# Kernel tuning notes

Hardware: AMD Instinct MI355X
Metric: run time of the kernel (lower is better)

The kernel has to match this reference:

```python
import jax, jax.numpy as jnp
import numpy as np

DELTA = 0.1      # delta from __init__
LN_EPS = 1e-5    # torch LayerNorm default eps

B, IN, OUT, E = 256, 512, 512, 256


def setup_inputs() -> dict:
    key = jax.random.key(0)
    ks = jax.random.split(key, 6)
    return {
        "x": jax.random.normal(ks[0], (B, IN), dtype=jnp.float32),
        # nn.init.normal_(std=0.1), shape (out_features, in_features)
        "weights": 0.1 * jax.random.normal(ks[1], (OUT, IN), dtype=jnp.float32),
        # frozen predicate embeddings (in_features, embedding_dim)
        "pred_emb": jax.random.normal(ks[2], (IN, E), dtype=jnp.float32),
        # nn.Linear(E, OUT): weight (OUT, E), bias (OUT,)
        "attn_w": jax.random.uniform(ks[3], (OUT, E), dtype=jnp.float32,
                                      minval=-1.0, maxval=1.0) / np.sqrt(E),
        "attn_b": jax.random.uniform(ks[4], (OUT,), dtype=jnp.float32,
                                      minval=-1.0, maxval=1.0) / np.sqrt(E),
        # nn.LayerNorm(OUT)
        "ln_g": jnp.ones((OUT,), dtype=jnp.float32),
        "ln_b": jnp.zeros((OUT,), dtype=jnp.float32),
    }


def _layernorm(s, g, b):
    mu = s.mean(axis=-1, keepdims=True)
    var = ((s - mu) ** 2).mean(axis=-1, keepdims=True)
    return (s - mu) * jax.lax.rsqrt(var + LN_EPS) * g + b


def reference(x, weights, pred_emb, attn_w, attn_b, ln_g, ln_b):
    # semantic attention gate: batch-invariant, compute once -> (IN, OUT)
    scores = pred_emb @ attn_w.T + attn_b                    # (IN, OUT)
    sig = jax.nn.sigmoid(_layernorm(scores, ln_g, ln_b))     # (IN, OUT)

    xe = x[:, :, None]                                       # (B, IN, 1)
    wt = weights.T[None]                                     # (1, IN, OUT)
    # abs_weight * attn_adjusted, fused elementwise -> (B, IN, OUT)
    aw = jnp.abs(xe * wt) * (sig[None] * xe)

    bias = aw.max(axis=1) - aw.sum(axis=1)                   # CONJUNCTION: max - sum
    return x @ weights.T + DELTA * bias                      # (B, OUT)
```

## Files before the change

kernel.cpp:

```cpp
#include <hip/hip_runtime.h>
#include <hip/hip_bf16.h>
#include <math.h>

#define B_   256
#define IN_  512
#define OUT_ 512
#define E_   256
#define DELTA_ 0.1f
#define LN_EPS_ 1e-5f

#define K1_R 2

__global__ __launch_bounds__(256)
void k1_scores_ln_sig(const float* __restrict__ pred_emb,
                      const float* __restrict__ attn_w,
                      const float* __restrict__ attn_b,
                      const float* __restrict__ ln_g,
                      const float* __restrict__ ln_b,
                      const float* __restrict__ weights,
                      float2* __restrict__ wv) {
    __shared__ float pe[K1_R][E_];
    __shared__ float red[4][K1_R][2];
    __shared__ float smu[K1_R], srs[K1_R];

    const int t    = threadIdx.x;
    const int lane = t & 63;
    const int wid  = t >> 6;
    const int i0   = blockIdx.x * K1_R;

    #pragma unroll
    for (int r = 0; r < K1_R; ++r)
        pe[r][t] = pred_emb[(size_t)(i0 + r) * E_ + t];
    __syncthreads();

    const float4 (*pe4)[E_ / 4] = reinterpret_cast<const float4(*)[E_ / 4]>(pe);

    float acc[K1_R][2];
    #pragma unroll
    for (int oo = 0; oo < 2; ++oo) {
        const int o = t + oo * 256;
        const float4* wrow = reinterpret_cast<const float4*>(attn_w + (size_t)o * E_);
        float a0 = 0.f, a1 = 0.f;
        #pragma unroll 8
        for (int e4 = 0; e4 < E_ / 4; ++e4) {
            float4 w4 = wrow[e4];
            float4 p0 = pe4[0][e4];
            float4 p1 = pe4[1][e4];
            a0 += p0.x * w4.x + p0.y * w4.y + p0.z * w4.z + p0.w * w4.w;
            a1 += p1.x * w4.x + p1.y * w4.y + p1.z * w4.z + p1.w * w4.w;
        }
        const float bo = attn_b[o];
        acc[0][oo] = a0 + bo;
        acc[1][oo] = a1 + bo;
    }

    #pragma unroll
    for (int r = 0; r < K1_R; ++r) {
        float s1 = acc[r][0] + acc[r][1];
        float s2 = acc[r][0] * acc[r][0] + acc[r][1] * acc[r][1];
        #pragma unroll
        for (int off = 32; off > 0; off >>= 1) {
            s1 += __shfl_down(s1, off);
            s2 += __shfl_down(s2, off);
        }
        if (lane == 0) { red[wid][r][0] = s1; red[wid][r][1] = s2; }
    }
    __syncthreads();
    if (t < K1_R) {
        float s1 = red[0][t][0] + red[1][t][0] + red[2][t][0] + red[3][t][0];
        float s2 = red[0][t][1] + red[1][t][1] + red[2][t][1] + red[3][t][1];
        float mu  = s1 / (float)OUT_;
        float var = s2 / (float)OUT_ - mu * mu;
        smu[t] = mu;
        srs[t] = rsqrtf(var + LN_EPS_);
    }
    __syncthreads();

    #pragma unroll
    for (int oo = 0; oo < 2; ++oo) {
        const int o = t + oo * 256;
        const float g  = ln_g[o];
        const float bb = ln_b[o];
        #pragma unroll
        for (int r = 0; r < K1_R; ++r) {
            float z  = (acc[r][oo] - smu[r]) * srs[r] * g + bb;
            float sg = 1.f / (1.f + expf(-z));
            float w  = weights[(size_t)o * IN_ + (i0 + r)];
            wv[(size_t)(i0 + r) * OUT_ + o] = make_float2(w, fabsf(w) * sg);
        }
    }
}

#define K2_SK 4
#define K2_CH 128
#define K2_BO (B_ * OUT_)

__global__ __launch_bounds__(256)
void k2_partials(const float* __restrict__ x,
                 const float2* __restrict__ wv,
                 float* __restrict__ plin,
                 float* __restrict__ pmax) {
    __shared__ float4 xs4[32 * 33];
    __shared__ float2 ws2[K2_CH * 17];

    const int t  = threadIdx.x;
    const int ot = t & 15;
    const int bl = t >> 4;
    const int o0 = blockIdx.x * 16;
    const int b0 = blockIdx.y * 32;
    const int sk = blockIdx.z;
    const int i0 = sk * K2_CH;

    #pragma unroll
    for (int k = 0; k < 4; ++k) {
        int p    = t + k * 256;
        int row  = p >> 5;
        int col4 = p & 31;
        xs4[row * 33 + col4] = reinterpret_cast<const float4*>(
            x + (size_t)(b0 + row) * IN_ + i0)[col4];
    }
    #pragma unroll
    for (int k = 0; k < 8; ++k) {
        int r = (t >> 4) + 16 * k;
        int c = t & 15;
        ws2[r * 17 + c] = wv[(size_t)(i0 + r) * OUT_ + o0 + c];
    }
    __syncthreads();

    const int o = o0 + ot;
    float da = 0.f, sa = 0.f, ma = -INFINITY;
    float db = 0.f, sb = 0.f, mb = -INFINITY;

    #pragma unroll 4
    for (int i4 = 0; i4 < K2_CH / 4; ++i4) {
        float4 xa = xs4[bl * 33 + i4];
        float4 xb = xs4[(bl + 16) * 33 + i4];
        float4 ua = make_float4(xa.x * fabsf(xa.x), xa.y * fabsf(xa.y),
                                xa.z * fabsf(xa.z), xa.w * fabsf(xa.w));
        float4 ub = make_float4(xb.x * fabsf(xb.x), xb.y * fabsf(xb.y),
                                xb.z * fabsf(xb.z), xb.w * fabsf(xb.w));
        float2 w0 = ws2[(4 * i4 + 0) * 17 + ot];
        float2 w1 = ws2[(4 * i4 + 1) * 17 + ot];
        float2 w2 = ws2[(4 * i4 + 2) * 17 + ot];
        float2 w3 = ws2[(4 * i4 + 3) * 17 + ot];
        float p;
        da = fmaf(xa.x, w0.x, da); p = ua.x * w0.y; sa += p; ma = fmaxf(ma, p);
        db = fmaf(xb.x, w0.x, db); p = ub.x * w0.y; sb += p; mb = fmaxf(mb, p);
        da = fmaf(xa.y, w1.x, da); p = ua.y * w1.y; sa += p; ma = fmaxf(ma, p);
        db = fmaf(xb.y, w1.x, db); p = ub.y * w1.y; sb += p; mb = fmaxf(mb, p);
        da = fmaf(xa.z, w2.x, da); p = ua.z * w2.y; sa += p; ma = fmaxf(ma, p);
        db = fmaf(xb.z, w2.x, db); p = ub.z * w2.y; sb += p; mb = fmaxf(mb, p);
        da = fmaf(xa.w, w3.x, da); p = ua.w * w3.y; sa += p; ma = fmaxf(ma, p);
        db = fmaf(xb.w, w3.x, db); p = ub.w * w3.y; sb += p; mb = fmaxf(mb, p);
    }

    const size_t boa = (size_t)(b0 + bl) * OUT_ + o;
    const size_t bob = boa + (size_t)16 * OUT_;
    plin[(size_t)sk * K2_BO + boa] = da - DELTA_ * sa;
    pmax[(size_t)sk * K2_BO + boa] = ma;
    plin[(size_t)sk * K2_BO + bob] = db - DELTA_ * sb;
    pmax[(size_t)sk * K2_BO + bob] = mb;
}

__global__ __launch_bounds__(256)
void k3_combine(const float* __restrict__ plin,
                const float* __restrict__ pmax,
                float* __restrict__ out) {
    const int g = blockIdx.x * 256 + threadIdx.x;
    float l = plin[g] + plin[K2_BO + g] + plin[2 * K2_BO + g] + plin[3 * K2_BO + g];
    float m = fmaxf(fmaxf(pmax[g], pmax[K2_BO + g]),
                    fmaxf(pmax[2 * K2_BO + g], pmax[3 * K2_BO + g]));
    out[g] = l + DELTA_ * m;
}

extern "C" void kernel_launch(void* const* d_in, const int* in_sizes, int n_in,
                              void* d_out, int out_size, void* d_ws, size_t ws_size,
                              hipStream_t stream) {
    const float* x        = (const float*)d_in[0];
    const float* weights  = (const float*)d_in[1];
    const float* pred_emb = (const float*)d_in[2];
    const float* attn_w   = (const float*)d_in[3];
    const float* attn_b   = (const float*)d_in[4];
    const float* ln_g     = (const float*)d_in[5];
    const float* ln_b     = (const float*)d_in[6];
    float* out = (float*)d_out;

    float2* wv   = (float2*)d_ws;
    float*  plin = (float*)d_ws + 2 * (size_t)IN_ * OUT_;
    float*  pmax = plin + (size_t)K2_SK * K2_BO;

    k1_scores_ln_sig<<<IN_ / K1_R, 256, 0, stream>>>(
        pred_emb, attn_w, attn_b, ln_g, ln_b, weights, wv);

    k2_partials<<<dim3(OUT_ / 16, B_ / 32, K2_SK), 256, 0, stream>>>(
        x, wv, plin, pmax);

    k3_combine<<<K2_BO / 256, 256, 0, stream>>>(plin, pmax, out);
}
```

Measured before the change: 101.4 us.

## Widen k1 to 512 threads, raise k2 batch tile to 64, vectorize combine

k1 now launches 512 threads per block, one output column per thread, and reads the two weight values as a single float2. k2 doubles its batch tile from 32 to 64 rows, so each thread keeps four row accumulators and each weight tile loaded into shared memory is reused across more rows. k3 reads and writes float4 to cut the number of memory instructions. The larger k2 tile halves the grid, which may reduce occupancy and raises register pressure.

```diff
diff --git a/kernel.cpp b/kernel.cpp
--- a/kernel.cpp
+++ b/kernel.cpp
@@ -9,9 +9,7 @@
 #define DELTA_ 0.1f
 #define LN_EPS_ 1e-5f
 
-#define K1_R 2
-
-__global__ __launch_bounds__(256)
+__global__ __launch_bounds__(512)
 void k1_scores_ln_sig(const float* __restrict__ pred_emb,
                       const float* __restrict__ attn_w,
                       const float* __restrict__ attn_b,
@@ -19,56 +17,56 @@
                       const float* __restrict__ ln_b,
                       const float* __restrict__ weights,
                       float2* __restrict__ wv) {
-    __shared__ float pe[K1_R][E_];
-    __shared__ float red[4][K1_R][2];
-    __shared__ float smu[K1_R], srs[K1_R];
+    __shared__ float pe[2][E_];
+    __shared__ float red[8][2][2];
+    __shared__ float smu[2], srs[2];
 
     const int t    = threadIdx.x;
     const int lane = t & 63;
     const int wid  = t >> 6;
-    const int i0   = blockIdx.x * K1_R;
-
-    #pragma unroll
-    for (int r = 0; r < K1_R; ++r)
-        pe[r][t] = pred_emb[(size_t)(i0 + r) * E_ + t];
-    __syncthreads();
-
-    const float4 (*pe4)[E_ / 4] = reinterpret_cast<const float4(*)[E_ / 4]>(pe);
-
-    float acc[K1_R][2];
-    #pragma unroll
-    for (int oo = 0; oo < 2; ++oo) {
-        const int o = t + oo * 256;
-        const float4* wrow = reinterpret_cast<const float4*>(attn_w + (size_t)o * E_);
-        float a0 = 0.f, a1 = 0.f;
-        #pragma unroll 8
-        for (int e4 = 0; e4 < E_ / 4; ++e4) {
-            float4 w4 = wrow[e4];
-            float4 p0 = pe4[0][e4];
-            float4 p1 = pe4[1][e4];
-            a0 += p0.x * w4.x + p0.y * w4.y + p0.z * w4.z + p0.w * w4.w;
-            a1 += p1.x * w4.x + p1.y * w4.y + p1.z * w4.z + p1.w * w4.w;
-        }
-        const float bo = attn_b[o];
-        acc[0][oo] = a0 + bo;
-        acc[1][oo] = a1 + bo;
-    }
-
-    #pragma unroll
-    for (int r = 0; r < K1_R; ++r) {
-        float s1 = acc[r][0] + acc[r][1];
-        float s2 = acc[r][0] * acc[r][0] + acc[r][1] * acc[r][1];
+    const int i0   = blockIdx.x * 2;
+    const int o    = t;
+
+    pe[t >> 8][t & 255] = pred_emb[(size_t)(i0 + (t >> 8)) * E_ + (t & 255)];
+    __syncthreads();
+
+    const float4* p0 = reinterpret_cast<const float4*>(pe[0]);
+    const float4* p1 = reinterpret_cast<const float4*>(pe[1]);
+    const float4* wrow = reinterpret_cast<const float4*>(attn_w + (size_t)o * E_);
+
+    float a0 = 0.f, a1 = 0.f;
+    #pragma unroll 8
+    for (int e4 = 0; e4 < E_ / 4; ++e4) {
+        float4 w4 = wrow[e4];
+        float4 q0 = p0[e4];
+        float4 q1 = p1[e4];
+        a0 += q0.x * w4.x + q0.y * w4.y + q0.z * w4.z + q0.w * w4.w;
+        a1 += q1.x * w4.x + q1.y * w4.y + q1.z * w4.z + q1.w * w4.w;
+    }
+    const float bo = attn_b[o];
+    a0 += bo;
+    a1 += bo;
+
+    {
+        float s1 = a0, s2 = a0 * a0;
+        float u1 = a1, u2 = a1 * a1;
         #pragma unroll
         for (int off = 32; off > 0; off >>= 1) {
             s1 += __shfl_down(s1, off);
             s2 += __shfl_down(s2, off);
+            u1 += __shfl_down(u1, off);
+            u2 += __shfl_down(u2, off);
         }
-        if (lane == 0) { red[wid][r][0] = s1; red[wid][r][1] = s2; }
-    }
-    __syncthreads();
-    if (t < K1_R) {
-        float s1 = red[0][t][0] + red[1][t][0] + red[2][t][0] + red[3][t][0];
-        float s2 = red[0][t][1] + red[1][t][1] + red[2][t][1] + red[3][t][1];
+        if (lane == 0) {
+            red[wid][0][0] = s1; red[wid][0][1] = s2;
+            red[wid][1][0] = u1; red[wid][1][1] = u2;
+        }
+    }
+    __syncthreads();
+    if (t < 2) {
+        float s1 = 0.f, s2 = 0.f;
+        #pragma unroll
+        for (int w = 0; w < 8; ++w) { s1 += red[w][t][0]; s2 += red[w][t][1]; }
         float mu  = s1 / (float)OUT_;
         float var = s2 / (float)OUT_ - mu * mu;
         smu[t] = mu;
@@ -76,19 +74,16 @@
     }
     __syncthreads();
 
-    #pragma unroll
-    for (int oo = 0; oo < 2; ++oo) {
-        const int o = t + oo * 256;
-        const float g  = ln_g[o];
-        const float bb = ln_b[o];
-        #pragma unroll
-        for (int r = 0; r < K1_R; ++r) {
-            float z  = (acc[r][oo] - smu[r]) * srs[r] * g + bb;
-            float sg = 1.f / (1.f + expf(-z));
-            float w  = weights[(size_t)o * IN_ + (i0 + r)];
-            wv[(size_t)(i0 + r) * OUT_ + o] = make_float2(w, fabsf(w) * sg);
-        }
-    }
+    const float g  = ln_g[o];
+    const float bb = ln_b[o];
+    float z0 = (a0 - smu[0]) * srs[0] * g + bb;
+    float z1 = (a1 - smu[1]) * srs[1] * g + bb;
+    float sg0 = 1.f / (1.f + expf(-z0));
+    float sg1 = 1.f / (1.f + expf(-z1));
+
+    float2 w01 = *reinterpret_cast<const float2*>(weights + (size_t)o * IN_ + i0);
+    wv[(size_t)(i0 + 0) * OUT_ + o] = make_float2(w01.x, fabsf(w01.x) * sg0);
+    wv[(size_t)(i0 + 1) * OUT_ + o] = make_float2(w01.y, fabsf(w01.y) * sg1);
 }
 
 #define K2_SK 4
@@ -100,19 +95,19 @@
                  const float2* __restrict__ wv,
                  float* __restrict__ plin,
                  float* __restrict__ pmax) {
-    __shared__ float4 xs4[32 * 33];
+    __shared__ float4 xs4[64 * 33];
     __shared__ float2 ws2[K2_CH * 17];
 
     const int t  = threadIdx.x;
     const int ot = t & 15;
     const int bl = t >> 4;
     const int o0 = blockIdx.x * 16;
-    const int b0 = blockIdx.y * 32;
+    const int b0 = blockIdx.y * 64;
     const int sk = blockIdx.z;
     const int i0 = sk * K2_CH;
 
     #pragma unroll
-    for (int k = 0; k < 4; ++k) {
+    for (int k = 0; k < 8; ++k) {
         int p    = t + k * 256;
         int row  = p >> 5;
         int col4 = p & 31;
@@ -121,56 +116,83 @@
     }
     #pragma unroll
     for (int k = 0; k < 8; ++k) {
-        int r = (t >> 4) + 16 * k;
-        int c = t & 15;
-        ws2[r * 17 + c] = wv[(size_t)(i0 + r) * OUT_ + o0 + c];
+        int r = bl + 16 * k;
+        ws2[r * 17 + ot] = wv[(size_t)(i0 + r) * OUT_ + o0 + ot];
     }
     __syncthreads();
 
     const int o = o0 + ot;
-    float da = 0.f, sa = 0.f, ma = -INFINITY;
-    float db = 0.f, sb = 0.f, mb = -INFINITY;
-
-    #pragma unroll 4
+    float d0 = 0.f, s0 = 0.f, m0 = -INFINITY;
+    float d1 = 0.f, s1 = 0.f, m1 = -INFINITY;
+    float d2 = 0.f, s2 = 0.f, m2 = -INFINITY;
+    float d3 = 0.f, s3 = 0.f, m3 = -INFINITY;
+
+    #pragma unroll 2
     for (int i4 = 0; i4 < K2_CH / 4; ++i4) {
-        float4 xa = xs4[bl * 33 + i4];
-        float4 xb = xs4[(bl + 16) * 33 + i4];
-        float4 ua = make_float4(xa.x * fabsf(xa.x), xa.y * fabsf(xa.y),
-                                xa.z * fabsf(xa.z), xa.w * fabsf(xa.w));
-        float4 ub = make_float4(xb.x * fabsf(xb.x), xb.y * fabsf(xb.y),
-                                xb.z * fabsf(xb.z), xb.w * fabsf(xb.w));
+        float4 x0 = xs4[(bl +  0) * 33 + i4];
+        float4 x1 = xs4[(bl + 16) * 33 + i4];
+        float4 x2 = xs4[(bl + 32) * 33 + i4];
+        float4 x3 = xs4[(bl + 48) * 33 + i4];
         float2 w0 = ws2[(4 * i4 + 0) * 17 + ot];
         float2 w1 = ws2[(4 * i4 + 1) * 17 + ot];
         float2 w2 = ws2[(4 * i4 + 2) * 17 + ot];
         float2 w3 = ws2[(4 * i4 + 3) * 17 + ot];
         float p;
-        da = fmaf(xa.x, w0.x, da); p = ua.x * w0.y; sa += p; ma = fmaxf(ma, p);
-        db = fmaf(xb.x, w0.x, db); p = ub.x * w0.y; sb += p; mb = fmaxf(mb, p);
-        da = fmaf(xa.y, w1.x, da); p = ua.y * w1.y; sa += p; ma = fmaxf(ma, p);
-        db = fmaf(xb.y, w1.x, db); p = ub.y * w1.y; sb += p; mb = fmaxf(mb, p);
-        da = fmaf(xa.z, w2.x, da); p = ua.z * w2.y; sa += p; ma = fmaxf(ma, p);
-        db = fmaf(xb.z, w2.x, db); p = ub.z * w2.y; sb += p; mb = fmaxf(mb, p);
-        da = fmaf(xa.w, w3.x, da); p = ua.w * w3.y; sa += p; ma = fmaxf(ma, p);
-        db = fmaf(xb.w, w3.x, db); p = ub.w * w3.y; sb += p; mb = fmaxf(mb, p);
-    }
-
-    const size_t boa = (size_t)(b0 + bl) * OUT_ + o;
-    const size_t bob = boa + (size_t)16 * OUT_;
-    plin[(size_t)sk * K2_BO + boa] = da - DELTA_ * sa;
-    pmax[(size_t)sk * K2_BO + boa] = ma;
-    plin[(size_t)sk * K2_BO + bob] = db - DELTA_ * sb;
-    pmax[(size_t)sk * K2_BO + bob] = mb;
+        float4 u0 = make_float4(x0.x * fabsf(x0.x), x0.y * fabsf(x0.y),
+                                x0.z * fabsf(x0.z), x0.w * fabsf(x0.w));
+        float4 u1 = make_float4(x1.x * fabsf(x1.x), x1.y * fabsf(x1.y),
+                                x1.z * fabsf(x1.z), x1.w * fabsf(x1.w));
+        float4 u2 = make_float4(x2.x * fabsf(x2.x), x2.y * fabsf(x2.y),
+                                x2.z * fabsf(x2.z), x2.w * fabsf(x2.w));
+        float4 u3 = make_float4(x3.x * fabsf(x3.x), x3.y * fabsf(x3.y),
+                                x3.z * fabsf(x3.z), x3.w * fabsf(x3.w));
+
+        d0 = fmaf(x0.x, w0.x, d0); p = u0.x * w0.y; s0 += p; m0 = fmaxf(m0, p);
+        d1 = fmaf(x1.x, w0.x, d1); p = u1.x * w0.y; s1 += p; m1 = fmaxf(m1, p);
+        d2 = fmaf(x2.x, w0.x, d2); p = u2.x * w0.y; s2 += p; m2 = fmaxf(m2, p);
+        d3 = fmaf(x3.x, w0.x, d3); p = u3.x * w0.y; s3 += p; m3 = fmaxf(m3, p);
+
+        d0 = fmaf(x0.y, w1.x, d0); p = u0.y * w1.y; s0 += p; m0 = fmaxf(m0, p);
+        d1 = fmaf(x1.y, w1.x, d1); p = u1.y * w1.y; s1 += p; m1 = fmaxf(m1, p);
+        d2 = fmaf(x2.y, w1.x, d2); p = u2.y * w1.y; s2 += p; m2 = fmaxf(m2, p);
+        d3 = fmaf(x3.y, w1.x, d3); p = u3.y * w1.y; s3 += p; m3 = fmaxf(m3, p);
+
+        d0 = fmaf(x0.z, w2.x, d0); p = u0.z * w2.y; s0 += p; m0 = fmaxf(m0, p);
+        d1 = fmaf(x1.z, w2.x, d1); p = u1.z * w2.y; s1 += p; m1 = fmaxf(m1, p);
+        d2 = fmaf(x2.z, w2.x, d2); p = u2.z * w2.y; s2 += p; m2 = fmaxf(m2, p);
+        d3 = fmaf(x3.z, w2.x, d3); p = u3.z * w2.y; s3 += p; m3 = fmaxf(m3, p);
+
+        d0 = fmaf(x0.w, w3.x, d0); p = u0.w * w3.y; s0 += p; m0 = fmaxf(m0, p);
+        d1 = fmaf(x1.w, w3.x, d1); p = u1.w * w3.y; s1 += p; m1 = fmaxf(m1, p);
+        d2 = fmaf(x2.w, w3.x, d2); p = u2.w * w3.y; s2 += p; m2 = fmaxf(m2, p);
+        d3 = fmaf(x3.w, w3.x, d3); p = u3.w * w3.y; s3 += p; m3 = fmaxf(m3, p);
+    }
+
+    const size_t base = (size_t)sk * K2_BO + (size_t)b0 * OUT_ + o;
+    plin[base + (size_t)(bl +  0) * OUT_] = d0 - DELTA_ * s0;
+    plin[base + (size_t)(bl + 16) * OUT_] = d1 - DELTA_ * s1;
+    plin[base + (size_t)(bl + 32) * OUT_] = d2 - DELTA_ * s2;
+    plin[base + (size_t)(bl + 48) * OUT_] = d3 - DELTA_ * s3;
+    pmax[base + (size_t)(bl +  0) * OUT_] = m0;
+    pmax[base + (size_t)(bl + 16) * OUT_] = m1;
+    pmax[base + (size_t)(bl + 32) * OUT_] = m2;
+    pmax[base + (size_t)(bl + 48) * OUT_] = m3;
 }
 
 __global__ __launch_bounds__(256)
-void k3_combine(const float* __restrict__ plin,
-                const float* __restrict__ pmax,
-                float* __restrict__ out) {
+void k3_combine(const float4* __restrict__ plin4,
+                const float4* __restrict__ pmax4,
+                float4* __restrict__ out4) {
     const int g = blockIdx.x * 256 + threadIdx.x;
-    float l = plin[g] + plin[K2_BO + g] + plin[2 * K2_BO + g] + plin[3 * K2_BO + g];
-    float m = fmaxf(fmaxf(pmax[g], pmax[K2_BO + g]),
-                    fmaxf(pmax[2 * K2_BO + g], pmax[3 * K2_BO + g]));
-    out[g] = l + DELTA_ * m;
+    const int Q = K2_BO / 4;
+    float4 l0 = plin4[g], l1 = plin4[Q + g], l2 = plin4[2 * Q + g], l3 = plin4[3 * Q + g];
+    float4 m0 = pmax4[g], m1 = pmax4[Q + g], m2 = pmax4[2 * Q + g], m3 = pmax4[3 * Q + g];
+    float4 r;
+    r.x = (l0.x + l1.x + l2.x + l3.x) + DELTA_ * fmaxf(fmaxf(m0.x, m1.x), fmaxf(m2.x, m3.x));
+    r.y = (l0.y + l1.y + l2.y + l3.y) + DELTA_ * fmaxf(fmaxf(m0.y, m1.y), fmaxf(m2.y, m3.y));
+    r.z = (l0.z + l1.z + l2.z + l3.z) + DELTA_ * fmaxf(fmaxf(m0.z, m1.z), fmaxf(m2.z, m3.z));
+    r.w = (l0.w + l1.w + l2.w + l3.w) + DELTA_ * fmaxf(fmaxf(m0.w, m1.w), fmaxf(m2.w, m3.w));
+    out4[g] = r;
 }
 
 extern "C" void kernel_launch(void* const* d_in, const int* in_sizes, int n_in,
@@ -183,17 +205,17 @@
     const float* attn_b   = (const float*)d_in[4];
     const float* ln_g     = (const float*)d_in[5];
     const float* ln_b     = (const float*)d_in[6];
-    float* out = (float*)d_out;
 
     float2* wv   = (float2*)d_ws;
     float*  plin = (float*)d_ws + 2 * (size_t)IN_ * OUT_;
     float*  pmax = plin + (size_t)K2_SK * K2_BO;
 
-    k1_scores_ln_sig<<<IN_ / K1_R, 256, 0, stream>>>(
+    k1_scores_ln_sig<<<IN_ / 2, 512, 0, stream>>>(
         pred_emb, attn_w, attn_b, ln_g, ln_b, weights, wv);
 
-    k2_partials<<<dim3(OUT_ / 16, B_ / 32, K2_SK), 256, 0, stream>>>(
+    k2_partials<<<dim3(OUT_ / 16, B_ / 64, K2_SK), 256, 0, stream>>>(
         x, wv, plin, pmax);
 
-    k3_combine<<<K2_BO / 256, 256, 0, stream>>>(plin, pmax, out);
-}
+    k3_combine<<<K2_BO / 4 / 256, 256, 0, stream>>>(
+        (const float4*)plin, (const float4*)pmax, (float4*)d_out);
+}
```

Result: no change. 99.59 us (-1.8%).
